# Kernel optimization log

Measured on AMD Instinct MI355X. Metric: run time of the kernel, lower is better.

The kernel has to match this reference:

```python
import jax, jax.numpy as jnp
import numpy as np

N, IN_DIM, MLPW, HID, NCLS = 2048, 1024, 16, 256, 4


def setup_inputs() -> dict:
    key = jax.random.key(0)
    ks = jax.random.split(key, 12)
    f32 = jnp.float32
    return {
        "x": jax.random.normal(ks[0], (N, IN_DIM), f32),
        "adj": jax.random.uniform(ks[1], (N, N), f32),
        "xdeg": jax.random.uniform(ks[2], (N, N), f32),
        "ydeg": jax.random.uniform(ks[3], (N, N), f32),
        # edge MLP([3, mlp_width, 2])
        "Wm1": jax.random.normal(ks[4], (3, MLPW), f32) * (1.0 / np.sqrt(3.0)),
        "bm1": jnp.zeros((MLPW,), f32),
        "Wm2": jax.random.normal(ks[5], (MLPW, 2), f32) * (1.0 / np.sqrt(MLPW)),
        "bm2": jnp.zeros((2,), f32),
        # GCN / dense layers (stored as [in, out]; torch Linear applies x @ W.T)
        "Wg1": jax.random.normal(ks[6], (IN_DIM, HID), f32) * (1.0 / np.sqrt(IN_DIM)),
        "Wl2": jax.random.normal(ks[7], (HID, 64), f32) * (1.0 / np.sqrt(HID)),
        "bl2": jnp.zeros((64,), f32),
        "Wg2": jax.random.normal(ks[8], (64, NCLS), f32) * (1.0 / 8.0),
    }


def reference(x, adj, xdeg, ydeg, Wm1, bm1, Wm2, bm2, Wg1, Wl2, bl2, Wg2):
    n = adj.shape[0]
    # Edge-feature MLP mask. The torch code gathers nonzero entries, runs the
    # MLP, scatters back into a zero buffer, then multiplies by adj. Computing
    # the mask densely is mathematically identical because adj * mask is zero
    # wherever adj is zero.
    feats = jnp.stack([adj, xdeg, ydeg], axis=-1)          # [N, N, 3]
    h = jax.nn.relu(feats @ Wm1 + bm1)                     # [N, N, MLPW]
    mask = jax.nn.softmax(h @ Wm2 + bm2, axis=-1)[..., 1]  # [N, N]
    A = adj * mask + jnp.eye(n, dtype=adj.dtype)
    # Symmetric-ish normalization: D_row^{-1/2} A D_col^{-1/2}
    # (the torch diag-matmul chain reduces to this row/col scaling).
    rowsum = jnp.sum(A, axis=1)
    colsum = jnp.sum(A, axis=0)
    dr = jnp.where(rowsum > 0, jax.lax.rsqrt(jnp.where(rowsum > 0, rowsum, 1.0)), 0.0)
    dc = jnp.where(colsum > 0, jax.lax.rsqrt(jnp.where(colsum > 0, colsum, 1.0)), 0.0)
    A = dr[:, None] * A * dc[None, :]
    # GCN layer 1 (dropout = identity in eval mode)
    hid = (A @ (x @ Wg1)) @ Wl2 + bl2                      # [N, 64]
    # GCN layer 2
    out = A @ (hid @ Wg2)                                  # [N, n_classes]
    return out, hid
```

## Files before the change

kernel.cpp:

```cpp
#include <hip/hip_runtime.h>

#define NN 2048
#define MLPW 16

typedef __attribute__((ext_vector_type(8))) short short8v;
typedef __attribute__((ext_vector_type(16))) float float16v;
typedef __attribute__((ext_vector_type(4))) unsigned short ushort4v;
typedef __attribute__((ext_vector_type(8))) unsigned short ushort8v;

__device__ __forceinline__ unsigned short f2b(float f) {
  unsigned int u = __float_as_uint(f);
  unsigned int r = (u + 0x7fffu + ((u >> 16) & 1u)) >> 16;
  return (unsigned short)r;
}
__device__ __forceinline__ float b2f(unsigned short u) {
  return __uint_as_float(((unsigned int)u) << 16);
}

__global__ void __launch_bounds__(256) edge_kernel(
    const float* __restrict__ adj, const float* __restrict__ xdeg,
    const float* __restrict__ ydeg,
    const float* __restrict__ Wm1, const float* __restrict__ bm1,
    const float* __restrict__ Wm2, const float* __restrict__ bm2,
    unsigned short* __restrict__ Abf, float* __restrict__ dr) {
  __shared__ float w1[48], b1[16], w2[32], b2s[2];
  __shared__ float wsum[4];
  const int tid = threadIdx.x;
  if (tid < 48) w1[tid] = Wm1[tid];
  if (tid < 16) b1[tid] = bm1[tid];
  if (tid < 32) w2[tid] = Wm2[tid];
  if (tid < 2) b2s[tid] = bm2[tid];
  __syncthreads();
  const int i = blockIdx.x;
  const float4* adj4 = (const float4*)(adj + (size_t)i * NN);
  const float4* xd4 = (const float4*)(xdeg + (size_t)i * NN);
  const float4* yd4 = (const float4*)(ydeg + (size_t)i * NN);
  ushort4v* A4 = (ushort4v*)(Abf + (size_t)i * NN);
  float rsum = 0.f;
  for (int j4 = tid; j4 < NN / 4; j4 += 256) {
    float4 av = adj4[j4], xv = xd4[j4], yv = yd4[j4];
    float aa[4] = {av.x, av.y, av.z, av.w};
    float xx[4] = {xv.x, xv.y, xv.z, xv.w};
    float yy[4] = {yv.x, yv.y, yv.z, yv.w};
    ushort4v oo;
#pragma unroll
    for (int e = 0; e < 4; e++) {
      float l0 = b2s[0], l1 = b2s[1];
#pragma unroll
      for (int k = 0; k < MLPW; k++) {
        float h = fmaf(aa[e], w1[k], fmaf(xx[e], w1[16 + k], fmaf(yy[e], w1[32 + k], b1[k])));
        h = fmaxf(h, 0.f);
        l0 = fmaf(h, w2[2 * k], l0);
        l1 = fmaf(h, w2[2 * k + 1], l1);
      }
      float mask = 1.f / (1.f + __expf(l0 - l1));
      float v = aa[e] * mask;
      int j = j4 * 4 + e;
      if (j == i) v += 1.f;
      oo[e] = f2b(v);
      rsum += v;
    }
    A4[j4] = oo;
  }
#pragma unroll
  for (int off = 32; off > 0; off >>= 1) rsum += __shfl_down(rsum, off);
  if ((tid & 63) == 0) wsum[tid >> 6] = rsum;
  __syncthreads();
  if (tid == 0) {
    float t = wsum[0] + wsum[1] + wsum[2] + wsum[3];
    dr[i] = t > 0.f ? rsqrtf(t) : 0.f;
  }
}

__global__ void __launch_bounds__(256) colsum_kernel(
    const unsigned short* __restrict__ Abf, float* __restrict__ partial) {
  const int j0 = threadIdx.x * 8;
  const int i0 = blockIdx.x * 64;
  float s[8] = {0, 0, 0, 0, 0, 0, 0, 0};
  for (int i = 0; i < 64; i++) {
    ushort8v a = *(const ushort8v*)&Abf[(size_t)(i0 + i) * NN + j0];
#pragma unroll
    for (int e = 0; e < 8; e++) s[e] += b2f(a[e]);
  }
  float* p = partial + (size_t)blockIdx.x * NN + j0;
  *(float4*)p = make_float4(s[0], s[1], s[2], s[3]);
  *(float4*)(p + 4) = make_float4(s[4], s[5], s[6], s[7]);
}

__global__ void __launch_bounds__(256) dc_kernel(
    const float* __restrict__ partial, float* __restrict__ dc) {
  const int j = blockIdx.x * 256 + threadIdx.x;
  float s = 0.f;
#pragma unroll
  for (int p = 0; p < 32; p++) s += partial[(size_t)p * NN + j];
  dc[j] = s > 0.f ? rsqrtf(s) : 0.f;
}

template <bool A_F32T, bool B_F32>
__global__ void __launch_bounds__(256) gemm_splitk_kernel(
    const void* __restrict__ Av, const void* __restrict__ Bv,
    float* __restrict__ P, int M, int N, int K, int Kc, int lda) {
  constexpr int SW = 136;
  __shared__ unsigned short As[32 * SW];
  __shared__ unsigned short Bs[128 * SW];
  const int tid = threadIdx.x;
  const int lane = tid & 63, wave = tid >> 6;
  const int l31 = lane & 31, half = lane >> 5;
  const int row0 = blockIdx.y * 32, col0 = blockIdx.x * 128;
  const int kbeg = blockIdx.z * Kc;

  float16v acc;
#pragma unroll
  for (int r = 0; r < 16; r++) acc[r] = 0.f;

  for (int k0 = 0; k0 < Kc; k0 += 128) {
    if (A_F32T) {
      const int kidx = tid >> 1, nh = (tid & 1) * 16;
      const float* src = (const float*)Av + (size_t)(kbeg + k0 + kidx) * lda + row0 + nh;
      float4 v0 = ((const float4*)src)[0], v1 = ((const float4*)src)[1];
      float4 v2 = ((const float4*)src)[2], v3 = ((const float4*)src)[3];
      const float vv[16] = {v0.x, v0.y, v0.z, v0.w, v1.x, v1.y, v1.z, v1.w,
                            v2.x, v2.y, v2.z, v2.w, v3.x, v3.y, v3.z, v3.w};
#pragma unroll
      for (int e = 0; e < 16; e++) As[(nh + e) * SW + kidx] = f2b(vv[e]);
    } else {
      const unsigned short* Ab = (const unsigned short*)Av;
#pragma unroll
      for (int i = 0; i < 2; i++) {
        const int id = tid + i * 256;
        const int r = id >> 4, c = id & 15;
        *(ushort8v*)&As[r * SW + c * 8] =
            *(const ushort8v*)&Ab[(size_t)(row0 + r) * K + kbeg + k0 + c * 8];
      }
    }
#pragma unroll
    for (int i = 0; i < 8; i++) {
      const int id = tid + i * 256;
      const int r = id >> 4, c = id & 15;
      if (B_F32) {
        const float* bp = (const float*)Bv + (size_t)(col0 + r) * K + kbeg + k0 + c * 8;
        float4 u = *(const float4*)bp, v = *(const float4*)(bp + 4);
        ushort8v pk = {f2b(u.x), f2b(u.y), f2b(u.z), f2b(u.w),
                       f2b(v.x), f2b(v.y), f2b(v.z), f2b(v.w)};
        *(ushort8v*)&Bs[r * SW + c * 8] = pk;
      } else {
        *(ushort8v*)&Bs[r * SW + c * 8] =
            *(const ushort8v*)&((const unsigned short*)Bv)[(size_t)(col0 + r) * K + kbeg + k0 + c * 8];
      }
    }
    __syncthreads();
#pragma unroll
    for (int ks = 0; ks < 8; ks++) {
      short8v a = *(const short8v*)&As[l31 * SW + ks * 16 + half * 8];
      short8v b = *(const short8v*)&Bs[(wave * 32 + l31) * SW + ks * 16 + half * 8];
      acc = __builtin_amdgcn_mfma_f32_32x32x16_bf16(a, b, acc, 0, 0, 0);
    }
    __syncthreads();
  }
  float* Pb = P + ((size_t)blockIdx.z * M + row0) * N + col0 + wave * 32 + l31;
#pragma unroll
  for (int reg = 0; reg < 16; reg++) {
    const int m = (reg & 3) + 8 * (reg >> 2) + 4 * half;
    Pb[(size_t)m * N] = acc[reg];
  }
}

__global__ void __launch_bounds__(256) reduce_xwt_kernel(
    const float* __restrict__ P, const float* __restrict__ dc,
    unsigned short* __restrict__ XWT) {
  const int t = blockIdx.x * 256 + threadIdx.x;
  const int i = t >> 8;
  const int j0 = (t & 255) * 8;
  float s[8] = {0, 0, 0, 0, 0, 0, 0, 0};
#pragma unroll
  for (int sk = 0; sk < 4; sk++) {
    const float* p = P + ((size_t)sk * 256 + i) * 2048 + j0;
    float4 u = *(const float4*)p, v = *(const float4*)(p + 4);
    s[0] += u.x; s[1] += u.y; s[2] += u.z; s[3] += u.w;
    s[4] += v.x; s[5] += v.y; s[6] += v.z; s[7] += v.w;
  }
  float4 d0 = *(const float4*)&dc[j0], d1 = *(const float4*)&dc[j0 + 4];
  ushort8v o = {f2b(s[0] * d0.x), f2b(s[1] * d0.y), f2b(s[2] * d0.z), f2b(s[3] * d0.w),
                f2b(s[4] * d1.x), f2b(s[5] * d1.y), f2b(s[6] * d1.z), f2b(s[7] * d1.w)};
  *(ushort8v*)&XWT[(size_t)i * 2048 + j0] = o;
}

__global__ void __launch_bounds__(256) tail_kernel(
    const float* __restrict__ P2, const float* __restrict__ dr,
    const float* __restrict__ dc, const float* __restrict__ Wl2,
    const float* __restrict__ bl2, const float* __restrict__ Wg2,
    float* __restrict__ hid, float* __restrict__ HW) {
  __shared__ float T1s[16][256];
  __shared__ float hidS[16][68];
  const int m0 = blockIdx.x * 16;
  const int tid = threadIdx.x;
#pragma unroll
  for (int i = 0; i < 16; i++) {
    const int idx = tid + i * 256;
    const int mi = idx >> 8, n = idx & 255;
    float s = 0.f;
#pragma unroll
    for (int sk = 0; sk < 4; sk++)
      s += P2[((size_t)sk * 2048 + m0 + mi) * 256 + n];
    T1s[mi][n] = s * dr[m0 + mi];
  }
  __syncthreads();
  const int j = tid & 63, mg = tid >> 6;
  float h[4] = {bl2[j], bl2[j], bl2[j], bl2[j]};
  for (int n = 0; n < 256; n++) {
    float w = Wl2[(size_t)n * 64 + j];
#pragma unroll
    for (int r = 0; r < 4; r++) h[r] = fmaf(T1s[mg * 4 + r][n], w, h[r]);
  }
#pragma unroll
  for (int r = 0; r < 4; r++) {
    hid[(size_t)(m0 + mg * 4 + r) * 64 + j] = h[r];
    hidS[mg * 4 + r][j] = h[r];
  }
  __syncthreads();
  if (tid < 64) {
    const int r = tid >> 2, c = tid & 3;
    float s = 0.f;
#pragma unroll
    for (int jj = 0; jj < 64; jj++) s = fmaf(hidS[r][jj], Wg2[jj * 4 + c], s);
    HW[(size_t)(m0 + r) * 4 + c] = s * dc[m0 + r];
  }
}

__global__ void __launch_bounds__(256) out_kernel(
    const unsigned short* __restrict__ Abf, const float* __restrict__ HW,
    const float* __restrict__ dr, float* __restrict__ outp) {
  const int i = blockIdx.x, tid = threadIdx.x;
  const ushort8v a8 = ((const ushort8v*)(Abf + (size_t)i * NN))[tid];
  const float4* hw4 = (const float4*)HW;
  const int j0 = tid * 8;
  float ax = 0.f, ay = 0.f, az = 0.f, aw = 0.f;
#pragma unroll
  for (int e = 0; e < 8; e++) {
    float a = b2f(a8[e]);
    float4 h = hw4[j0 + e];
    ax = fmaf(a, h.x, ax);
    ay = fmaf(a, h.y, ay);
    az = fmaf(a, h.z, az);
    aw = fmaf(a, h.w, aw);
  }
  __shared__ float red[4][256];
  red[0][tid] = ax; red[1][tid] = ay; red[2][tid] = az; red[3][tid] = aw;
  __syncthreads();
  for (int s = 128; s > 0; s >>= 1) {
    if (tid < s) {
      red[0][tid] += red[0][tid + s];
      red[1][tid] += red[1][tid + s];
      red[2][tid] += red[2][tid + s];
      red[3][tid] += red[3][tid + s];
    }
    __syncthreads();
  }
  if (tid < 4) outp[(size_t)i * 4 + tid] = dr[i] * red[tid][0];
}

extern "C" void kernel_launch(void* const* d_in, const int* in_sizes, int n_in,
                              void* d_out, int out_size, void* d_ws, size_t ws_size,
                              hipStream_t stream) {
  const float* x    = (const float*)d_in[0];
  const float* adj  = (const float*)d_in[1];
  const float* xdeg = (const float*)d_in[2];
  const float* ydeg = (const float*)d_in[3];
  const float* Wm1  = (const float*)d_in[4];
  const float* bm1  = (const float*)d_in[5];
  const float* Wm2  = (const float*)d_in[6];
  const float* bm2  = (const float*)d_in[7];
  const float* Wg1  = (const float*)d_in[8];
  const float* Wl2  = (const float*)d_in[9];
  const float* bl2  = (const float*)d_in[10];
  const float* Wg2  = (const float*)d_in[11];

  char* ws = (char*)d_ws;
  unsigned short* Abf  = (unsigned short*)(ws);
  unsigned short* XWT  = (unsigned short*)(ws + 8388608);
  float* P    = (float*)(ws + 9437184);
  float* part = (float*)(ws + 18350080);
  float* dr   = (float*)(ws + 18612224);
  float* dc   = (float*)(ws + 18620416);
  float* HW   = (float*)(ws + 18628608);

  float* outp = (float*)d_out;
  float* hid  = (float*)d_out + 2048 * 4;

  edge_kernel<<<NN, 256, 0, stream>>>(adj, xdeg, ydeg, Wm1, bm1, Wm2, bm2, Abf, dr);
  colsum_kernel<<<32, 256, 0, stream>>>(Abf, part);
  dc_kernel<<<NN / 256, 256, 0, stream>>>(part, dc);
  gemm_splitk_kernel<true, true><<<dim3(2048 / 128, 256 / 32, 4), 256, 0, stream>>>(
      Wg1, x, P, 256, 2048, 1024, 256, 256);
  reduce_xwt_kernel<<<256, 256, 0, stream>>>(P, dc, XWT);
  gemm_splitk_kernel<false, false><<<dim3(256 / 128, 2048 / 32, 4), 256, 0, stream>>>(
      Abf, XWT, P, 2048, 256, 2048, 512, 0);
  tail_kernel<<<2048 / 16, 256, 0, stream>>>(P, dr, dc, Wl2, bl2, Wg2, hid, HW);
  out_kernel<<<NN, 256, 0, stream>>>(Abf, HW, dr, outp);
}
```

Baseline: 178.3 us.

## Pre-convert GEMM inputs to bf16, enlarge GEMM tiles, raise split-K, widen reductions

A new aux kernel merges the column-sum partials (now 256 blocks instead of 32) with a one-time bf16 conversion of x and a transposed bf16 copy of Wg1. This removes the fp32-to-bf16 conversion and the strided transposed loads from the GEMM inner loop. The GEMM tile grows to 64x128 with two MFMA accumulators per wave, and split-K goes from 4 to 8, with the reduce and tail kernels adjusted to match. The dc and out kernels switch to wider parallel reductions (a shared-memory two-stage sum and wave shuffles). The cost is more workspace and twice as many split-K partials to write and read back.

```diff
diff --git a/kernel.cpp b/kernel.cpp
--- a/kernel.cpp
+++ b/kernel.cpp
@@ -72,96 +72,107 @@
   }
 }
 
-__global__ void __launch_bounds__(256) colsum_kernel(
-    const unsigned short* __restrict__ Abf, float* __restrict__ partial) {
-  const int j0 = threadIdx.x * 8;
-  const int i0 = blockIdx.x * 64;
-  float s[8] = {0, 0, 0, 0, 0, 0, 0, 0};
-  for (int i = 0; i < 64; i++) {
-    ushort8v a = *(const ushort8v*)&Abf[(size_t)(i0 + i) * NN + j0];
-#pragma unroll
-    for (int e = 0; e < 8; e++) s[e] += b2f(a[e]);
-  }
-  float* p = partial + (size_t)blockIdx.x * NN + j0;
-  *(float4*)p = make_float4(s[0], s[1], s[2], s[3]);
-  *(float4*)(p + 4) = make_float4(s[4], s[5], s[6], s[7]);
+__global__ void __launch_bounds__(256) aux_kernel(
+    const unsigned short* __restrict__ Abf, const float* __restrict__ x,
+    const float* __restrict__ Wg1, float* __restrict__ partial,
+    unsigned short* __restrict__ xb, unsigned short* __restrict__ Wg1T) {
+  const int b = blockIdx.x, tid = threadIdx.x;
+  if (b < 256) {
+    const int j0 = tid * 8, i0 = b * 8;
+    float s[8] = {0, 0, 0, 0, 0, 0, 0, 0};
+#pragma unroll
+    for (int i = 0; i < 8; i++) {
+      ushort8v a = *(const ushort8v*)&Abf[(size_t)(i0 + i) * NN + j0];
+#pragma unroll
+      for (int e = 0; e < 8; e++) s[e] += b2f(a[e]);
+    }
+    float* p = partial + (size_t)b * NN + j0;
+    *(float4*)p = make_float4(s[0], s[1], s[2], s[3]);
+    *(float4*)(p + 4) = make_float4(s[4], s[5], s[6], s[7]);
+  } else if (b < 1280) {
+    const size_t idx = (size_t)(b - 256) * 2048 + (size_t)tid * 8;
+    const float4 u = *(const float4*)&x[idx], v = *(const float4*)&x[idx + 4];
+    ushort8v o = {f2b(u.x), f2b(u.y), f2b(u.z), f2b(u.w),
+                  f2b(v.x), f2b(v.y), f2b(v.z), f2b(v.w)};
+    *(ushort8v*)&xb[idx] = o;
+  } else {
+    const int bo = b - 1280;
+    const int n = bo * 2 + (tid >> 7);
+    const int k0 = (tid & 127) * 8;
+    ushort8v o;
+#pragma unroll
+    for (int e = 0; e < 8; e++) o[e] = f2b(Wg1[(size_t)(k0 + e) * 256 + n]);
+    *(ushort8v*)&Wg1T[(size_t)n * 1024 + k0] = o;
+  }
 }
 
 __global__ void __launch_bounds__(256) dc_kernel(
     const float* __restrict__ partial, float* __restrict__ dc) {
-  const int j = blockIdx.x * 256 + threadIdx.x;
+  __shared__ float red[8][32];
+  const int l = threadIdx.x & 31, g = threadIdx.x >> 5;
+  const int col = blockIdx.x * 32 + l;
   float s = 0.f;
 #pragma unroll
-  for (int p = 0; p < 32; p++) s += partial[(size_t)p * NN + j];
-  dc[j] = s > 0.f ? rsqrtf(s) : 0.f;
-}
-
-template <bool A_F32T, bool B_F32>
+  for (int q = 0; q < 32; q++) s += partial[(size_t)(g * 32 + q) * NN + col];
+  red[g][l] = s;
+  __syncthreads();
+  if (g == 0) {
+    float t = s;
+#pragma unroll
+    for (int gg = 1; gg < 8; gg++) t += red[gg][l];
+    dc[col] = t > 0.f ? rsqrtf(t) : 0.f;
+  }
+}
+
 __global__ void __launch_bounds__(256) gemm_splitk_kernel(
-    const void* __restrict__ Av, const void* __restrict__ Bv,
-    float* __restrict__ P, int M, int N, int K, int Kc, int lda) {
+    const unsigned short* __restrict__ A, const unsigned short* __restrict__ B,
+    float* __restrict__ P, int M, int N, int K, int Kc) {
   constexpr int SW = 136;
-  __shared__ unsigned short As[32 * SW];
+  __shared__ unsigned short As[64 * SW];
   __shared__ unsigned short Bs[128 * SW];
   const int tid = threadIdx.x;
   const int lane = tid & 63, wave = tid >> 6;
   const int l31 = lane & 31, half = lane >> 5;
-  const int row0 = blockIdx.y * 32, col0 = blockIdx.x * 128;
+  const int mh = wave & 1, nh = wave >> 1;
+  const int row0 = blockIdx.y * 64, col0 = blockIdx.x * 128;
   const int kbeg = blockIdx.z * Kc;
 
-  float16v acc;
-#pragma unroll
-  for (int r = 0; r < 16; r++) acc[r] = 0.f;
+  float16v acc0, acc1;
+#pragma unroll
+  for (int r = 0; r < 16; r++) { acc0[r] = 0.f; acc1[r] = 0.f; }
 
   for (int k0 = 0; k0 < Kc; k0 += 128) {
-    if (A_F32T) {
-      const int kidx = tid >> 1, nh = (tid & 1) * 16;
-      const float* src = (const float*)Av + (size_t)(kbeg + k0 + kidx) * lda + row0 + nh;
-      float4 v0 = ((const float4*)src)[0], v1 = ((const float4*)src)[1];
-      float4 v2 = ((const float4*)src)[2], v3 = ((const float4*)src)[3];
-      const float vv[16] = {v0.x, v0.y, v0.z, v0.w, v1.x, v1.y, v1.z, v1.w,
-                            v2.x, v2.y, v2.z, v2.w, v3.x, v3.y, v3.z, v3.w};
-#pragma unroll
-      for (int e = 0; e < 16; e++) As[(nh + e) * SW + kidx] = f2b(vv[e]);
-    } else {
-      const unsigned short* Ab = (const unsigned short*)Av;
-#pragma unroll
-      for (int i = 0; i < 2; i++) {
-        const int id = tid + i * 256;
-        const int r = id >> 4, c = id & 15;
-        *(ushort8v*)&As[r * SW + c * 8] =
-            *(const ushort8v*)&Ab[(size_t)(row0 + r) * K + kbeg + k0 + c * 8];
-      }
+#pragma unroll
+    for (int i = 0; i < 4; i++) {
+      const int id = tid + i * 256;
+      const int r = id >> 4, c = id & 15;
+      *(ushort8v*)&As[r * SW + c * 8] =
+          *(const ushort8v*)&A[(size_t)(row0 + r) * K + kbeg + k0 + c * 8];
     }
 #pragma unroll
     for (int i = 0; i < 8; i++) {
       const int id = tid + i * 256;
       const int r = id >> 4, c = id & 15;
-      if (B_F32) {
-        const float* bp = (const float*)Bv + (size_t)(col0 + r) * K + kbeg + k0 + c * 8;
-        float4 u = *(const float4*)bp, v = *(const float4*)(bp + 4);
-        ushort8v pk = {f2b(u.x), f2b(u.y), f2b(u.z), f2b(u.w),
-                       f2b(v.x), f2b(v.y), f2b(v.z), f2b(v.w)};
-        *(ushort8v*)&Bs[r * SW + c * 8] = pk;
-      } else {
-        *(ushort8v*)&Bs[r * SW + c * 8] =
-            *(const ushort8v*)&((const unsigned short*)Bv)[(size_t)(col0 + r) * K + kbeg + k0 + c * 8];
-      }
+      *(ushort8v*)&Bs[r * SW + c * 8] =
+          *(const ushort8v*)&B[(size_t)(col0 + r) * K + kbeg + k0 + c * 8];
     }
     __syncthreads();
 #pragma unroll
     for (int ks = 0; ks < 8; ks++) {
-      short8v a = *(const short8v*)&As[l31 * SW + ks * 16 + half * 8];
-      short8v b = *(const short8v*)&Bs[(wave * 32 + l31) * SW + ks * 16 + half * 8];
-      acc = __builtin_amdgcn_mfma_f32_32x32x16_bf16(a, b, acc, 0, 0, 0);
+      short8v a = *(const short8v*)&As[(mh * 32 + l31) * SW + ks * 16 + half * 8];
+      short8v b0 = *(const short8v*)&Bs[(nh * 64 + l31) * SW + ks * 16 + half * 8];
+      short8v b1 = *(const short8v*)&Bs[(nh * 64 + 32 + l31) * SW + ks * 16 + half * 8];
+      acc0 = __builtin_amdgcn_mfma_f32_32x32x16_bf16(a, b0, acc0, 0, 0, 0);
+      acc1 = __builtin_amdgcn_mfma_f32_32x32x16_bf16(a, b1, acc1, 0, 0, 0);
     }
     __syncthreads();
   }
-  float* Pb = P + ((size_t)blockIdx.z * M + row0) * N + col0 + wave * 32 + l31;
+  float* Pb = P + ((size_t)blockIdx.z * M + row0 + mh * 32) * N + col0 + nh * 64 + l31;
 #pragma unroll
   for (int reg = 0; reg < 16; reg++) {
     const int m = (reg & 3) + 8 * (reg >> 2) + 4 * half;
-    Pb[(size_t)m * N] = acc[reg];
+    Pb[(size_t)m * N] = acc0[reg];
+    Pb[(size_t)m * N + 32] = acc1[reg];
   }
 }
 
@@ -173,7 +184,7 @@
   const int j0 = (t & 255) * 8;
   float s[8] = {0, 0, 0, 0, 0, 0, 0, 0};
 #pragma unroll
-  for (int sk = 0; sk < 4; sk++) {
+  for (int sk = 0; sk < 8; sk++) {
     const float* p = P + ((size_t)sk * 256 + i) * 2048 + j0;
     float4 u = *(const float4*)p, v = *(const float4*)(p + 4);
     s[0] += u.x; s[1] += u.y; s[2] += u.z; s[3] += u.w;
@@ -190,35 +201,34 @@
     const float* __restrict__ dc, const float* __restrict__ Wl2,
     const float* __restrict__ bl2, const float* __restrict__ Wg2,
     float* __restrict__ hid, float* __restrict__ HW) {
-  __shared__ float T1s[16][256];
-  __shared__ float hidS[16][68];
-  const int m0 = blockIdx.x * 16;
+  __shared__ float T1s[8][256];
+  __shared__ float hidS[8][68];
+  const int m0 = blockIdx.x * 8;
   const int tid = threadIdx.x;
 #pragma unroll
-  for (int i = 0; i < 16; i++) {
+  for (int i = 0; i < 8; i++) {
     const int idx = tid + i * 256;
     const int mi = idx >> 8, n = idx & 255;
     float s = 0.f;
 #pragma unroll
-    for (int sk = 0; sk < 4; sk++)
+    for (int sk = 0; sk < 8; sk++)
       s += P2[((size_t)sk * 2048 + m0 + mi) * 256 + n];
     T1s[mi][n] = s * dr[m0 + mi];
   }
   __syncthreads();
   const int j = tid & 63, mg = tid >> 6;
-  float h[4] = {bl2[j], bl2[j], bl2[j], bl2[j]};
+  float h0 = bl2[j], h1 = h0;
   for (int n = 0; n < 256; n++) {
     float w = Wl2[(size_t)n * 64 + j];
-#pragma unroll
-    for (int r = 0; r < 4; r++) h[r] = fmaf(T1s[mg * 4 + r][n], w, h[r]);
-  }
-#pragma unroll
-  for (int r = 0; r < 4; r++) {
-    hid[(size_t)(m0 + mg * 4 + r) * 64 + j] = h[r];
-    hidS[mg * 4 + r][j] = h[r];
-  }
-  __syncthreads();
-  if (tid < 64) {
+    h0 = fmaf(T1s[mg * 2 + 0][n], w, h0);
+    h1 = fmaf(T1s[mg * 2 + 1][n], w, h1);
+  }
+  hid[(size_t)(m0 + mg * 2 + 0) * 64 + j] = h0;
+  hid[(size_t)(m0 + mg * 2 + 1) * 64 + j] = h1;
+  hidS[mg * 2 + 0][j] = h0;
+  hidS[mg * 2 + 1][j] = h1;
+  __syncthreads();
+  if (tid < 32) {
     const int r = tid >> 2, c = tid & 3;
     float s = 0.f;
 #pragma unroll
@@ -244,19 +254,22 @@
     az = fmaf(a, h.z, az);
     aw = fmaf(a, h.w, aw);
   }
-  __shared__ float red[4][256];
-  red[0][tid] = ax; red[1][tid] = ay; red[2][tid] = az; red[3][tid] = aw;
-  __syncthreads();
-  for (int s = 128; s > 0; s >>= 1) {
-    if (tid < s) {
-      red[0][tid] += red[0][tid + s];
-      red[1][tid] += red[1][tid + s];
-      red[2][tid] += red[2][tid + s];
-      red[3][tid] += red[3][tid + s];
-    }
-    __syncthreads();
-  }
-  if (tid < 4) outp[(size_t)i * 4 + tid] = dr[i] * red[tid][0];
+#pragma unroll
+  for (int off = 32; off > 0; off >>= 1) {
+    ax += __shfl_down(ax, off);
+    ay += __shfl_down(ay, off);
+    az += __shfl_down(az, off);
+    aw += __shfl_down(aw, off);
+  }
+  __shared__ float wsum[4][4];
+  const int w = tid >> 6;
+  if ((tid & 63) == 0) {
+    wsum[w][0] = ax; wsum[w][1] = ay; wsum[w][2] = az; wsum[w][3] = aw;
+  }
+  __syncthreads();
+  if (tid < 4)
+    outp[(size_t)i * 4 + tid] =
+        dr[i] * (wsum[0][tid] + wsum[1][tid] + wsum[2][tid] + wsum[3][tid]);
 }
 
 extern "C" void kernel_launch(void* const* d_in, const int* in_sizes, int n_in,
@@ -278,23 +291,25 @@
   char* ws = (char*)d_ws;
   unsigned short* Abf  = (unsigned short*)(ws);
   unsigned short* XWT  = (unsigned short*)(ws + 8388608);
-  float* P    = (float*)(ws + 9437184);
-  float* part = (float*)(ws + 18350080);
-  float* dr   = (float*)(ws + 18612224);
-  float* dc   = (float*)(ws + 18620416);
-  float* HW   = (float*)(ws + 18628608);
+  float* P     = (float*)(ws + 9437184);
+  float* part  = (float*)(ws + 26214400);
+  unsigned short* xb   = (unsigned short*)(ws + 28311552);
+  unsigned short* Wg1T = (unsigned short*)(ws + 32505856);
+  float* dr    = (float*)(ws + 33030144);
+  float* dc    = (float*)(ws + 33038336);
+  float* HW    = (float*)(ws + 33046528);
 
   float* outp = (float*)d_out;
   float* hid  = (float*)d_out + 2048 * 4;
 
   edge_kernel<<<NN, 256, 0, stream>>>(adj, xdeg, ydeg, Wm1, bm1, Wm2, bm2, Abf, dr);
-  colsum_kernel<<<32, 256, 0, stream>>>(Abf, part);
-  dc_kernel<<<NN / 256, 256, 0, stream>>>(part, dc);
-  gemm_splitk_kernel<true, true><<<dim3(2048 / 128, 256 / 32, 4), 256, 0, stream>>>(
-      Wg1, x, P, 256, 2048, 1024, 256, 256);
+  aux_kernel<<<1408, 256, 0, stream>>>(Abf, x, Wg1, part, xb, Wg1T);
+  dc_kernel<<<64, 256, 0, stream>>>(part, dc);
+  gemm_splitk_kernel<<<dim3(2048 / 128, 256 / 64, 8), 256, 0, stream>>>(
+      Wg1T, xb, P, 256, 2048, 1024, 128);
   reduce_xwt_kernel<<<256, 256, 0, stream>>>(P, dc, XWT);
-  gemm_splitk_kernel<false, false><<<dim3(256 / 128, 2048 / 32, 4), 256, 0, stream>>>(
-      Abf, XWT, P, 2048, 256, 2048, 512, 0);
-  tail_kernel<<<2048 / 16, 256, 0, stream>>>(P, dr, dc, Wl2, bl2, Wg2, hid, HW);
+  gemm_splitk_kernel<<<dim3(256 / 128, 2048 / 64, 8), 256, 0, stream>>>(
+      Abf, XWT, P, 2048, 256, 2048, 256);
+  tail_kernel<<<2048 / 8, 256, 0, stream>>>(P, dr, dc, Wl2, bl2, Wg2, hid, HW);
   out_kernel<<<NN, 256, 0, stream>>>(Abf, HW, dr, outp);
 }
```

Result: faster. 172.6 us (-3.2%).
